# Performance work log

Hardware: AMD Instinct MI355X
Metric: run time of the kernel (lower is better)

Reference implementation:

```python
import jax, jax.numpy as jnp
import numpy as np
import math

EMBED = 1024
HEADS = 16
HEAD_DIM = EMBED // HEADS
WINDOW = 128
B, S = 2, 2048


def setup_inputs() -> dict:
    key = jax.random.key(0)
    k1, k2, k3, k4 = jax.random.split(key, 4)
    values = jax.random.normal(k1, (B, S, EMBED), dtype=jnp.float32)
    keys = jax.random.normal(k2, (B, S, EMBED), dtype=jnp.float32)
    queries = jax.random.normal(k3, (B, S, EMBED), dtype=jnp.float32)
    # sliding-window band mask: 1 where |i-j| <= WINDOW//2, else 0
    idx = jnp.arange(S)
    band = (jnp.abs(idx[:, None] - idx[None, :]) <= WINDOW // 2).astype(jnp.int32)
    mask = band[None, None, :, :]  # [1,1,S,S], broadcasts over batch and heads
    w_out = jax.random.normal(k4, (EMBED, EMBED), dtype=jnp.float32) * (1.0 / math.sqrt(EMBED))
    b_out = jnp.zeros((EMBED,), dtype=jnp.float32)
    return {"values": values, "keys": keys, "queries": queries, "mask": mask,
            "w_out": w_out, "b_out": b_out}


def reference(values, keys, queries, mask, w_out, b_out):
    N, q_len = queries.shape[0], queries.shape[1]
    v = values.reshape(N, -1, HEADS, HEAD_DIM)
    k = keys.reshape(N, -1, HEADS, HEAD_DIM)
    q = queries.reshape(N, -1, HEADS, HEAD_DIM)
    # dense N x N energy, as in the original (no windowed blocking)
    energy = jnp.einsum('nqhd,nkhd->nhqk', q, k)
    energy = jnp.where(mask == 0, jnp.float32(-1e20), energy)
    attn = jax.nn.softmax(energy / math.sqrt(EMBED), axis=3)
    out = jnp.einsum('nhql,nlhd->nqhd', attn, v).reshape(N, q_len, HEADS * HEAD_DIM)
    return out @ w_out.T + b_out
```

## Files before the change

kernel.cpp:

```cpp
#include <hip/hip_runtime.h>

typedef __bf16 bf16x8 __attribute__((ext_vector_type(8)));
typedef float floatx4 __attribute__((ext_vector_type(4)));
typedef unsigned short ushortx8 __attribute__((ext_vector_type(8)));
typedef unsigned short ushortx4 __attribute__((ext_vector_type(4)));
typedef unsigned short ushort_t;

#define SB 2048
#define EB 1024
#define HB 16
#define DB 64
#define QT 128
#define KB2 256
#define KROW 72
#define VROW 272
#define PROW 168
#define XROW 72

__device__ __forceinline__ ushort_t f2bf(float f) {
    union { float f; unsigned int u; } v; v.f = f;
    unsigned int r = v.u + 0x7fffu + ((v.u >> 16) & 1u);
    return (ushort_t)(r >> 16);
}

union BF8 { ushortx8 u; bf16x8 b; };

__global__ __launch_bounds__(256) void cvtw_kernel(const float* __restrict__ w,
                                                   ushort_t* __restrict__ wb) {
    int i = blockIdx.x * 256 + threadIdx.x;
    const float4 v = ((const float4*)w)[i];
    ushortx4 o;
    o.x = f2bf(v.x); o.y = f2bf(v.y); o.z = f2bf(v.z); o.w = f2bf(v.w);
    ((ushortx4*)wb)[i] = o;
}

__global__ __launch_bounds__(512) void attn_kernel(const float* __restrict__ Vg,
                                                   const float* __restrict__ Kg,
                                                   const float* __restrict__ Qg,
                                                   ushort_t* __restrict__ Xg) {
    __shared__ ushort_t KP[8 * 16 * PROW];
    __shared__ ushort_t Vt[DB * VROW];

    const int tid  = threadIdx.x;
    const int wave = tid >> 6;
    const int lane = tid & 63;
    const int l15  = lane & 15;
    const int l4   = lane >> 4;

    const int qt = blockIdx.x & 15;
    const int h  = (blockIdx.x >> 4) & 15;
    const int b  = blockIdx.x >> 8;

    const int q0     = qt * QT;
    const int kstart = q0 - 64;

    const float* Kbase = Kg + ((size_t)b * SB) * EB + h * DB;
    const float* Vbase = Vg + ((size_t)b * SB) * EB + h * DB;

    #pragma unroll
    for (int it = 0; it < (KB2 * DB / 4) / 512; ++it) {
        int idx = it * 512 + tid;
        int j   = idx >> 4;
        int d4  = (idx & 15) * 4;
        int kk  = kstart + j;
        float4 kv = make_float4(0.f, 0.f, 0.f, 0.f);
        float4 vv = make_float4(0.f, 0.f, 0.f, 0.f);
        if (kk >= 0 && kk < SB) {
            kv = *(const float4*)(Kbase + (size_t)kk * EB + d4);
            vv = *(const float4*)(Vbase + (size_t)kk * EB + d4);
        }
        ushortx4 ku;
        ku.x = f2bf(kv.x); ku.y = f2bf(kv.y); ku.z = f2bf(kv.z); ku.w = f2bf(kv.w);
        *(ushortx4*)(KP + j * KROW + d4) = ku;
        int cs = ((((j >> 3) ^ (l15 & 7)) << 3) | (j & 7));
        Vt[(d4 + 0) * VROW + cs] = f2bf(vv.x);
        Vt[(d4 + 1) * VROW + cs] = f2bf(vv.y);
        Vt[(d4 + 2) * VROW + cs] = f2bf(vv.z);
        Vt[(d4 + 3) * VROW + cs] = f2bf(vv.w);
    }
    {
        int r = tid >> 3, c = 256 + ((tid & 7) * 2);
        if (r < DB) { Vt[r * VROW + c] = 0; Vt[r * VROW + c + 1] = 0; }
    }

    const int qrow = q0 + wave * 16 + l15;
    const float* Qrow = Qg + ((size_t)b * SB + qrow) * EB + h * DB;
    bf16x8 qfrag[2];
    #pragma unroll
    for (int ks = 0; ks < 2; ++ks) {
        const float4* p = (const float4*)(Qrow + ks * 32 + l4 * 8);
        float4 a0 = p[0], a1 = p[1];
        BF8 t;
        t.u[0] = f2bf(a0.x); t.u[1] = f2bf(a0.y); t.u[2] = f2bf(a0.z); t.u[3] = f2bf(a0.w);
        t.u[4] = f2bf(a1.x); t.u[5] = f2bf(a1.y); t.u[6] = f2bf(a1.z); t.u[7] = f2bf(a1.w);
        qfrag[ks] = t.b;
    }

    __syncthreads();

    floatx4 sfrag[9];
    #pragma unroll
    for (int nt = 0; nt < 9; ++nt) {
        floatx4 acc = {0.f, 0.f, 0.f, 0.f};
        #pragma unroll
        for (int ks = 0; ks < 2; ++ks) {
            bf16x8 kf = *(const bf16x8*)(KP + (16 * (wave + nt) + l15) * KROW + ks * 32 + l4 * 8);
            acc = __builtin_amdgcn_mfma_f32_16x16x32_bf16(qfrag[ks], kf, acc, 0, 0, 0);
        }
        sfrag[nt] = acc;
    }

    const float scale2 = 0.04508421903306637f;
    #pragma unroll
    for (int nt = 0; nt < 9; ++nt) {
        int key = kstart + 16 * (wave + nt) + l15;
        #pragma unroll
        for (int r = 0; r < 4; ++r) {
            int m = l4 * 4 + r;
            int d = 16 * nt + l15 - m;
            bool valid = (d >= 0) && (d <= 128) && (key >= 0) && (key < SB);
            float s = sfrag[nt][r] * scale2;
            sfrag[nt][r] = valid ? s : -1e30f;
        }
    }
    #pragma unroll
    for (int r = 0; r < 4; ++r) {
        float mx = -1e30f;
        #pragma unroll
        for (int nt = 0; nt < 9; ++nt) mx = fmaxf(mx, sfrag[nt][r]);
        mx = fmaxf(mx, __shfl_xor(mx, 1));
        mx = fmaxf(mx, __shfl_xor(mx, 2));
        mx = fmaxf(mx, __shfl_xor(mx, 4));
        mx = fmaxf(mx, __shfl_xor(mx, 8));
        float sum = 0.f;
        #pragma unroll
        for (int nt = 0; nt < 9; ++nt) {
            float e = exp2f(sfrag[nt][r] - mx);
            sfrag[nt][r] = e;
            sum += e;
        }
        sum += __shfl_xor(sum, 1);
        sum += __shfl_xor(sum, 2);
        sum += __shfl_xor(sum, 4);
        sum += __shfl_xor(sum, 8);
        float inv = 1.f / sum;
        #pragma unroll
        for (int nt = 0; nt < 9; ++nt) sfrag[nt][r] *= inv;
    }

    __syncthreads();
    ushort_t* Pw = KP + wave * (16 * PROW);
    #pragma unroll
    for (int nt = 0; nt < 9; ++nt)
        #pragma unroll
        for (int r = 0; r < 4; ++r)
            Pw[(l4 * 4 + r) * PROW + nt * 16 + l15] = f2bf(sfrag[nt][r]);
    #pragma unroll
    for (int r = 0; r < 4; ++r) {
        int row = l4 * 4 + r;
        if (l15 < 12) {
            Pw[row * PROW + 144 + l15 * 2]     = 0;
            Pw[row * PROW + 144 + l15 * 2 + 1] = 0;
        }
    }

    floatx4 oacc[4];
    #pragma unroll
    for (int nt = 0; nt < 4; ++nt) {
        floatx4 acc = {0.f, 0.f, 0.f, 0.f};
        int dsw = (nt * 4 + (l15 >> 2)) & 7;
        #pragma unroll
        for (int ks = 0; ks < 5; ++ks) {
            int col = 16 * wave + ks * 32 + l4 * 8;
            int c   = col >> 3;
            int coff = (c < 32) ? ((c ^ dsw) << 3) : (c << 3);
            bf16x8 pf = *(const bf16x8*)(Pw + l15 * PROW + ks * 32 + l4 * 8);
            bf16x8 vf = *(const bf16x8*)(Vt + (nt * 16 + l15) * VROW + coff);
            acc = __builtin_amdgcn_mfma_f32_16x16x32_bf16(pf, vf, acc, 0, 0, 0);
        }
        oacc[nt] = acc;
    }

    __syncthreads();
    ushort_t* Xs = KP;
    #pragma unroll
    for (int nt = 0; nt < 4; ++nt)
        #pragma unroll
        for (int r = 0; r < 4; ++r)
            Xs[(wave * 16 + l4 * 4 + r) * XROW + nt * 16 + l15] = f2bf(oacc[nt][r]);
    __syncthreads();
    #pragma unroll
    for (int it = 0; it < 2; ++it) {
        int idx = it * 512 + tid;
        int row = idx >> 3, ch = idx & 7;
        bf16x8 val = *(const bf16x8*)(Xs + row * XROW + ch * 8);
        *(bf16x8*)(Xg + ((size_t)b * SB + q0 + row) * EB + h * DB + ch * 8) = val;
    }
}

__device__ __forceinline__ void async_load16(const void* g, void* l) {
    __builtin_amdgcn_global_load_lds((__attribute__((address_space(1))) void*)g,
                                     (__attribute__((address_space(3))) void*)l,
                                     16, 0, 0);
}

__global__ __launch_bounds__(128) void proj_kernel(const ushort_t* __restrict__ X,
                                                   const ushort_t* __restrict__ Wb,
                                                   const float* __restrict__ bias,
                                                   float* __restrict__ out) {
    __shared__ ushort_t As[128 * 64];
    __shared__ ushort_t Bs[64 * 64];

    const int tid  = threadIdx.x;
    const int wave = tid >> 6;
    const int lane = tid & 63;
    const int l15  = lane & 15;
    const int l4   = lane >> 4;

    const int m0 = blockIdx.x * 128;
    const int n0 = blockIdx.y * 64;
    const int wm = wave * 64;

    floatx4 acc[4][4];
    #pragma unroll
    for (int i = 0; i < 4; ++i)
        #pragma unroll
        for (int j = 0; j < 4; ++j)
            acc[i][j] = (floatx4){0.f, 0.f, 0.f, 0.f};

    const int kc8 = (((tid & 7) ^ ((tid >> 3) & 7)) << 3);
    const ushort_t* gA = X  + (size_t)(m0 + (tid >> 3)) * EB + kc8;
    const ushort_t* gB = Wb + (size_t)(n0 + (tid >> 3)) * EB + kc8;
    ushort_t* lA = As + wave * 512;
    ushort_t* lB = Bs + wave * 512;

    for (int kt = 0; kt < EB / 64; ++kt) {
        #pragma unroll
        for (int p = 0; p < 8; ++p) async_load16(gA + (size_t)p * 16 * EB, lA + p * 1024);
        #pragma unroll
        for (int p = 0; p < 4; ++p) async_load16(gB + (size_t)p * 16 * EB, lB + p * 1024);
        gA += 64; gB += 64;
        __syncthreads();

        #pragma unroll
        for (int ks = 0; ks < 2; ++ks) {
            const int sw = (((ks * 4 + l4) ^ (l15 & 7)) << 3);
            bf16x8 af[4], bfr[4];
            #pragma unroll
            for (int i = 0; i < 4; ++i)
                af[i] = *(const bf16x8*)(As + (wm + i * 16 + l15) * 64 + sw);
            #pragma unroll
            for (int j = 0; j < 4; ++j)
                bfr[j] = *(const bf16x8*)(Bs + (j * 16 + l15) * 64 + sw);
            #pragma unroll
            for (int i = 0; i < 4; ++i)
                #pragma unroll
                for (int j = 0; j < 4; ++j)
                    acc[i][j] = __builtin_amdgcn_mfma_f32_16x16x32_bf16(af[i], bfr[j], acc[i][j], 0, 0, 0);
        }
        __syncthreads();
    }

    #pragma unroll
    for (int j = 0; j < 4; ++j) {
        int col = n0 + j * 16 + l15;
        float bv = bias[col];
        #pragma unroll
        for (int i = 0; i < 4; ++i)
            #pragma unroll
            for (int r = 0; r < 4; ++r) {
                int row = m0 + wm + i * 16 + l4 * 4 + r;
                out[(size_t)row * EB + col] = acc[i][j][r] + bv;
            }
    }
}

extern "C" void kernel_launch(void* const* d_in, const int* in_sizes, int n_in,
                              void* d_out, int out_size, void* d_ws, size_t ws_size,
                              hipStream_t stream) {
    const float* values  = (const float*)d_in[0];
    const float* keys    = (const float*)d_in[1];
    const float* queries = (const float*)d_in[2];
    const float* w_out   = (const float*)d_in[4];
    const float* b_out   = (const float*)d_in[5];
    float* out = (float*)d_out;

    ushort_t* Xb = (ushort_t*)d_ws;
    ushort_t* Wb = (ushort_t*)d_ws + (size_t)4096 * 1024;

    cvtw_kernel<<<(EB * EB / 4) / 256, 256, 0, stream>>>(w_out, Wb);
    attn_kernel<<<2 * HB * (SB / QT), 512, 0, stream>>>(values, keys, queries, Xb);
    proj_kernel<<<dim3(4096 / 128, EB / 64), 128, 0, stream>>>(Xb, Wb, b_out, out);
}
```

Measured before the change: 137.8 us.

## Fold weight conversion into attention kernel and double-buffer projection GEMM

Removes the separate weight-conversion launch by having each attention block convert one slice of w_out (512 blocks x 512 float4 covers the whole 1024x1024 matrix). The projection GEMM becomes single-wave 64x64 tiles with double-buffered LDS, prefetching the next K-tile via async global-to-LDS loads and ordering them with vmcnt waits instead of barriers. This cuts one launch and hides load latency in the GEMM, but the smaller tiles reload operands more often and the hand-coded waitcnt values must be right for correctness.

```diff
diff --git a/kernel.cpp b/kernel.cpp
--- a/kernel.cpp
+++ b/kernel.cpp
@@ -25,18 +25,11 @@
 
 union BF8 { ushortx8 u; bf16x8 b; };
 
-__global__ __launch_bounds__(256) void cvtw_kernel(const float* __restrict__ w,
-                                                   ushort_t* __restrict__ wb) {
-    int i = blockIdx.x * 256 + threadIdx.x;
-    const float4 v = ((const float4*)w)[i];
-    ushortx4 o;
-    o.x = f2bf(v.x); o.y = f2bf(v.y); o.z = f2bf(v.z); o.w = f2bf(v.w);
-    ((ushortx4*)wb)[i] = o;
-}
-
 __global__ __launch_bounds__(512) void attn_kernel(const float* __restrict__ Vg,
                                                    const float* __restrict__ Kg,
                                                    const float* __restrict__ Qg,
+                                                   const float* __restrict__ Wg,
+                                                   ushort_t* __restrict__ Wb,
                                                    ushort_t* __restrict__ Xg) {
     __shared__ ushort_t KP[8 * 16 * PROW];
     __shared__ ushort_t Vt[DB * VROW];
@@ -46,6 +39,14 @@
     const int lane = tid & 63;
     const int l15  = lane & 15;
     const int l4   = lane >> 4;
+
+    {
+        int i = blockIdx.x * 512 + tid;
+        const float4 v = ((const float4*)Wg)[i];
+        ushortx4 o;
+        o.x = f2bf(v.x); o.y = f2bf(v.y); o.z = f2bf(v.z); o.w = f2bf(v.w);
+        ((ushortx4*)Wb)[i] = o;
+    }
 
     const int qt = blockIdx.x & 15;
     const int h  = (blockIdx.x >> 4) & 15;
@@ -204,22 +205,19 @@
                                      16, 0, 0);
 }
 
-__global__ __launch_bounds__(128) void proj_kernel(const ushort_t* __restrict__ X,
-                                                   const ushort_t* __restrict__ Wb,
-                                                   const float* __restrict__ bias,
-                                                   float* __restrict__ out) {
-    __shared__ ushort_t As[128 * 64];
-    __shared__ ushort_t Bs[64 * 64];
-
-    const int tid  = threadIdx.x;
-    const int wave = tid >> 6;
-    const int lane = tid & 63;
+__global__ __launch_bounds__(64) void proj_kernel(const ushort_t* __restrict__ X,
+                                                  const ushort_t* __restrict__ Wb,
+                                                  const float* __restrict__ bias,
+                                                  float* __restrict__ out) {
+    __shared__ ushort_t As[2][64 * 64];
+    __shared__ ushort_t Bs[2][64 * 64];
+
+    const int lane = threadIdx.x;
     const int l15  = lane & 15;
     const int l4   = lane >> 4;
 
-    const int m0 = blockIdx.x * 128;
+    const int m0 = blockIdx.x * 64;
     const int n0 = blockIdx.y * 64;
-    const int wm = wave * 64;
 
     floatx4 acc[4][4];
     #pragma unroll
@@ -228,19 +226,28 @@
         for (int j = 0; j < 4; ++j)
             acc[i][j] = (floatx4){0.f, 0.f, 0.f, 0.f};
 
-    const int kc8 = (((tid & 7) ^ ((tid >> 3) & 7)) << 3);
-    const ushort_t* gA = X  + (size_t)(m0 + (tid >> 3)) * EB + kc8;
-    const ushort_t* gB = Wb + (size_t)(n0 + (tid >> 3)) * EB + kc8;
-    ushort_t* lA = As + wave * 512;
-    ushort_t* lB = Bs + wave * 512;
+    const int kc8 = (((lane & 7) ^ ((lane >> 3) & 7)) << 3);
+    const ushort_t* gA = X  + (size_t)(m0 + (lane >> 3)) * EB + kc8;
+    const ushort_t* gB = Wb + (size_t)(n0 + (lane >> 3)) * EB + kc8;
+
+    #pragma unroll
+    for (int p = 0; p < 8; ++p) async_load16(gA + (size_t)p * 8 * EB, &As[0][p * 512]);
+    #pragma unroll
+    for (int p = 0; p < 8; ++p) async_load16(gB + (size_t)p * 8 * EB, &Bs[0][p * 512]);
 
     for (int kt = 0; kt < EB / 64; ++kt) {
-        #pragma unroll
-        for (int p = 0; p < 8; ++p) async_load16(gA + (size_t)p * 16 * EB, lA + p * 1024);
-        #pragma unroll
-        for (int p = 0; p < 4; ++p) async_load16(gB + (size_t)p * 16 * EB, lB + p * 1024);
-        gA += 64; gB += 64;
-        __syncthreads();
+        const int cur = kt & 1, nxt = cur ^ 1;
+        if (kt < EB / 64 - 1) {
+            const ushort_t* nA = gA + (kt + 1) * 64;
+            const ushort_t* nB = gB + (kt + 1) * 64;
+            #pragma unroll
+            for (int p = 0; p < 8; ++p) async_load16(nA + (size_t)p * 8 * EB, &As[nxt][p * 512]);
+            #pragma unroll
+            for (int p = 0; p < 8; ++p) async_load16(nB + (size_t)p * 8 * EB, &Bs[nxt][p * 512]);
+            __builtin_amdgcn_s_waitcnt(0x4F70);
+        } else {
+            __builtin_amdgcn_s_waitcnt(0x0F70);
+        }
 
         #pragma unroll
         for (int ks = 0; ks < 2; ++ks) {
@@ -248,17 +255,16 @@
             bf16x8 af[4], bfr[4];
             #pragma unroll
             for (int i = 0; i < 4; ++i)
-                af[i] = *(const bf16x8*)(As + (wm + i * 16 + l15) * 64 + sw);
+                af[i] = *(const bf16x8*)(&As[cur][(i * 16 + l15) * 64 + sw]);
             #pragma unroll
             for (int j = 0; j < 4; ++j)
-                bfr[j] = *(const bf16x8*)(Bs + (j * 16 + l15) * 64 + sw);
+                bfr[j] = *(const bf16x8*)(&Bs[cur][(j * 16 + l15) * 64 + sw]);
             #pragma unroll
             for (int i = 0; i < 4; ++i)
                 #pragma unroll
                 for (int j = 0; j < 4; ++j)
                     acc[i][j] = __builtin_amdgcn_mfma_f32_16x16x32_bf16(af[i], bfr[j], acc[i][j], 0, 0, 0);
         }
-        __syncthreads();
     }
 
     #pragma unroll
@@ -269,7 +275,7 @@
         for (int i = 0; i < 4; ++i)
             #pragma unroll
             for (int r = 0; r < 4; ++r) {
-                int row = m0 + wm + i * 16 + l4 * 4 + r;
+                int row = m0 + i * 16 + l4 * 4 + r;
                 out[(size_t)row * EB + col] = acc[i][j][r] + bv;
             }
     }
@@ -288,7 +294,6 @@
     ushort_t* Xb = (ushort_t*)d_ws;
     ushort_t* Wb = (ushort_t*)d_ws + (size_t)4096 * 1024;
 
-    cvtw_kernel<<<(EB * EB / 4) / 256, 256, 0, stream>>>(w_out, Wb);
-    attn_kernel<<<2 * HB * (SB / QT), 512, 0, stream>>>(values, keys, queries, Xb);
-    proj_kernel<<<dim3(4096 / 128, EB / 64), 128, 0, stream>>>(Xb, Wb, b_out, out);
-}
+    attn_kernel<<<2 * HB * (SB / QT), 512, 0, stream>>>(values, keys, queries, w_out, Wb, Xb);
+    proj_kernel<<<dim3(4096 / 64, EB / 64), 64, 0, stream>>>(Xb, Wb, b_out, out);
+}
```

After: 134.4 us. 2.5% less time.
